# Kernel tuning notes

Measured on AMD Instinct MI355X. Metric: run time of the kernel, lower is better.

Reference implementation:

```python
import jax, jax.numpy as jnp
import numpy as np

DIM = 256
NUM_LAYERS = 64


def setup_inputs() -> dict:
    key = jax.random.key(0)
    kx, kt = jax.random.split(key)
    x = jax.random.normal(kx, (32768, DIM), dtype=jnp.float32)
    # theta[l, p]: scalar angle for pair p in layer l. Odd-offset layers use only
    # the first DIM//2 - 1 entries. Matches torch.randn(()) * pi init.
    theta = jax.random.normal(kt, (NUM_LAYERS, DIM // 2), dtype=jnp.float32) * jnp.pi
    return {"x": x, "theta": theta}


def _apply_layer(x, th, offset):
    """Apply one layer of 2x2 Givens-like rotations to pairs (i, i+1).

    U = [[c, s], [s, -c]] with c=cos(2*theta), s=sin(2*theta); U is symmetric so
    out = vec @ U.T = vec @ U -> yi = c*xi + s*xj, yj = s*xi - c*xj.
    """
    b, d = x.shape
    if offset == 0:
        npairs = d // 2
        c = jnp.cos(2.0 * th[:npairs])  # [npairs]
        s = jnp.sin(2.0 * th[:npairs])
        v = x.reshape(b, npairs, 2)
        xi, xj = v[..., 0], v[..., 1]
        yi = c * xi + s * xj
        yj = s * xi - c * xj
        return jnp.stack([yi, yj], axis=-1).reshape(b, d)
    else:
        npairs = d // 2 - 1
        c = jnp.cos(2.0 * th[:npairs])
        s = jnp.sin(2.0 * th[:npairs])
        inner = x[:, 1:d - 1].reshape(b, npairs, 2)
        xi, xj = inner[..., 0], inner[..., 1]
        yi = c * xi + s * xj
        yj = s * xi - c * xj
        mid = jnp.stack([yi, yj], axis=-1).reshape(b, d - 2)
        return jnp.concatenate([x[:, :1], mid, x[:, d - 1:]], axis=1)


def reference(x, theta):
    # Python loop over num_layers (fixed, small structural set).
    for depth in range(NUM_LAYERS):
        x = _apply_layer(x, theta[depth], depth % 2)
    return x
```

## Files before the change

### kernel.cpp

```cpp
#include <hip/hip_runtime.h>
#include <math.h>

#define DIM 256
#define NLAYERS 64

typedef __attribute__((ext_vector_type(8))) short short8;
typedef __attribute__((ext_vector_type(4))) float f32x4;

__device__ __forceinline__ float dpp_shl1_zero(float v) {
    int r = __builtin_amdgcn_update_dpp(0, __float_as_int(v), 0x130, 0xF, 0xF, true);
    return __int_as_float(r);
}
__device__ __forceinline__ float dpp_shr1_keep(float oldv, float v) {
    int r = __builtin_amdgcn_update_dpp(__float_as_int(oldv), __float_as_int(v), 0x138, 0xF, 0xF, false);
    return __int_as_float(r);
}
__device__ __forceinline__ unsigned short f2bf(float f) {
    unsigned u = __float_as_uint(f);
    u += 0x7FFFu + ((u >> 16) & 1u);
    return (unsigned short)(u >> 16);
}

__global__ __launch_bounds__(1024)
void build_m_kernel(const float* __restrict__ theta, unsigned short* __restrict__ bfrag) {
    __shared__ float tbl[NLAYERS * DIM];
    const int tid = threadIdx.x;
    #pragma unroll
    for (int kk = 0; kk < 8; ++kk) {
        int idx = tid + 1024 * kk;
        int l = idx >> 7, p = idx & 127;
        float s, c;
        sincosf(2.0f * theta[idx], &s, &c);
        if ((l & 1) && (p == 127)) { c = 1.0f; s = 0.0f; }
        tbl[idx * 2 + 0] = c;
        tbl[idx * 2 + 1] = s;
    }
    __syncthreads();

    const int w = tid >> 6;
    const int t = tid & 63;
    const int row = blockIdx.x * 16 + w;

    float e[4];
    #pragma unroll
    for (int j = 0; j < 4; ++j) e[j] = (4 * t + j == row) ? 1.0f : 0.0f;

    const float4* tbl4 = (const float4*)tbl;
    #pragma unroll 2
    for (int l = 0; l < NLAYERS; l += 2) {
        float4 cs = tbl4[(l << 6) + t];
        {
            float a0 = e[0], a1 = e[1], a2 = e[2], a3 = e[3];
            e[0] = cs.x * a0 + cs.y * a1;
            e[1] = cs.y * a0 - cs.x * a1;
            e[2] = cs.z * a2 + cs.w * a3;
            e[3] = cs.w * a2 - cs.z * a3;
        }
        float4 cs1 = tbl4[((l + 1) << 6) + t];
        {
            float a1 = e[1], a2 = e[2], a3 = e[3];
            float n1 = cs1.x * a1 + cs1.y * a2;
            float n2 = cs1.y * a1 - cs1.x * a2;
            float xjn = dpp_shl1_zero(e[0]);
            float n3  = cs1.z * a3 + cs1.w * xjn;
            float snd = cs1.w * a3 - cs1.z * xjn;
            e[0] = dpp_shr1_keep(e[0], snd);
            e[1] = n1; e[2] = n2; e[3] = n3;
        }
    }

    const int kt = row >> 5, g8 = (row >> 3) & 3, ki = row & 7;
    #pragma unroll
    for (int j = 0; j < 4; ++j) {
        int col = 4 * t + j;
        bfrag[(((col >> 4) * 8 + kt) * 64 + g8 * 16 + (col & 15)) * 8 + ki] = f2bf(e[j]);
    }
}

__global__ __launch_bounds__(512, 4)
void clements_gemm(const float* __restrict__ x,
                   const unsigned short* __restrict__ bfrag,
                   float* __restrict__ out) {
    __shared__ unsigned short afrag[2][4096];

    const int tid = threadIdx.x;
    const int w   = tid >> 6;
    const int t   = tid & 63;
    const int l16 = t & 15;
    const int g   = t >> 4;
    const long rowbase = (long)blockIdx.x * 64;

    const int sr  = tid >> 5;
    const int seg = tid & 31;
    const int q   = seg >> 2;
    const int sg  = seg & 3;
    const int wslot = (q * 64 + ((sg * 16 + sr) ^ q)) * 8;
    const float* xp = x + (rowbase + sr) * 256 + seg * 8;

    f32x4 pref[4][2];
#define LOADC(i) { pref[i][0] = *(const f32x4*)(xp + (i) * 16 * 256);      \
                   pref[i][1] = *(const f32x4*)(xp + (i) * 16 * 256 + 4); }
#define WRITEC(i) { short8 h;                                              \
        h[0]=f2bf(pref[i][0][0]); h[1]=f2bf(pref[i][0][1]);                \
        h[2]=f2bf(pref[i][0][2]); h[3]=f2bf(pref[i][0][3]);                \
        h[4]=f2bf(pref[i][1][0]); h[5]=f2bf(pref[i][1][1]);                \
        h[6]=f2bf(pref[i][1][2]); h[7]=f2bf(pref[i][1][3]);                \
        *(short8*)&afrag[(i) & 1][wslot] = h; }

    LOADC(0)
    LOADC(1)

    short8 Bf[8][2];
    {
        const short8* bp = (const short8*)bfrag;
        #pragma unroll
        for (int nt = 0; nt < 2; ++nt)
            #pragma unroll
            for (int kt = 0; kt < 8; ++kt)
                Bf[kt][nt] = bp[((w * 2 + nt) * 8 + kt) * 64 + t];
    }

    WRITEC(0)
    __syncthreads();

    #pragma unroll
    for (int i = 0; i < 4; ++i) {
        if (i + 2 < 4) LOADC(i + 2)

        f32x4 a0 = {0.f,0.f,0.f,0.f}, a1 = {0.f,0.f,0.f,0.f};
        #pragma unroll
        for (int kt = 0; kt < 8; ++kt) {
            short8 A = *(const short8*)&afrag[i & 1][(kt * 64 + (t ^ kt)) * 8];
            a0 = __builtin_amdgcn_mfma_f32_16x16x32_bf16(A, Bf[kt][0], a0, 0, 0, 0);
            a1 = __builtin_amdgcn_mfma_f32_16x16x32_bf16(A, Bf[kt][1], a1, 0, 0, 0);
        }
        float* o = out + (rowbase + i * 16 + g * 4) * 256 + 32 * w + l16;
        #pragma unroll
        for (int j = 0; j < 4; ++j) {
            o[(long)j * 256 +  0] = a0[j];
            o[(long)j * 256 + 16] = a1[j];
        }

        if (i + 1 < 4) { WRITEC(i + 1) __syncthreads(); }
    }
#undef LOADC
#undef WRITEC
}

__global__ __launch_bounds__(1024, 4)
void clements_direct(const float* __restrict__ x,
                     const float* __restrict__ theta,
                     float* __restrict__ out) {
    __shared__ float tbl[NLAYERS * DIM];
    const int tid = threadIdx.x;
    #pragma unroll
    for (int k = 0; k < 8; ++k) {
        int idx = tid + 1024 * k;
        int l = idx >> 7;
        int p = idx & 127;
        float s, c;
        sincosf(2.0f * theta[idx], &s, &c);
        if ((l & 1) && (p == 127)) { c = 1.0f; s = 0.0f; }
        tbl[idx * 2 + 0] = c;
        tbl[idx * 2 + 1] = s;
    }
    __syncthreads();
    const int w = tid >> 6;
    const int t = tid & 63;
    const long base = ((long)blockIdx.x * 16 + w) * 8;
    float e[8][4];
    #pragma unroll
    for (int r = 0; r < 8; ++r) {
        float4 v = ((const float4*)(x + (base + r) * (long)DIM))[t];
        e[r][0] = v.x; e[r][1] = v.y; e[r][2] = v.z; e[r][3] = v.w;
    }
    const float4* tbl4 = (const float4*)tbl;
    #pragma unroll 2
    for (int l = 0; l < NLAYERS; l += 2) {
        float4 cs = tbl4[(l << 6) + t];
        #pragma unroll
        for (int r = 0; r < 8; ++r) {
            float a0 = e[r][0], a1 = e[r][1], a2 = e[r][2], a3 = e[r][3];
            e[r][0] = cs.x * a0 + cs.y * a1;
            e[r][1] = cs.y * a0 - cs.x * a1;
            e[r][2] = cs.z * a2 + cs.w * a3;
            e[r][3] = cs.w * a2 - cs.z * a3;
        }
        float4 cs1 = tbl4[((l + 1) << 6) + t];
        #pragma unroll
        for (int r = 0; r < 8; ++r) {
            float a1 = e[r][1], a2 = e[r][2], a3 = e[r][3];
            float n1 = cs1.x * a1 + cs1.y * a2;
            float n2 = cs1.y * a1 - cs1.x * a2;
            float xjn = dpp_shl1_zero(e[r][0]);
            float n3  = cs1.z * a3 + cs1.w * xjn;
            float snd = cs1.w * a3 - cs1.z * xjn;
            e[r][0] = dpp_shr1_keep(e[r][0], snd);
            e[r][1] = n1; e[r][2] = n2; e[r][3] = n3;
        }
    }
    #pragma unroll
    for (int r = 0; r < 8; ++r) {
        float4 v;
        v.x = e[r][0]; v.y = e[r][1]; v.z = e[r][2]; v.w = e[r][3];
        ((float4*)(out + (base + r) * (long)DIM))[t] = v;
    }
}

extern "C" void kernel_launch(void* const* d_in, const int* in_sizes, int n_in,
                              void* d_out, int out_size, void* d_ws, size_t ws_size,
                              hipStream_t stream) {
    const float* x     = (const float*)d_in[0];
    const float* theta = (const float*)d_in[1];
    float* out = (float*)d_out;

    const size_t need = (size_t)DIM * DIM * sizeof(unsigned short);
    if (ws_size >= need) {
        unsigned short* bfrag = (unsigned short*)d_ws;
        hipLaunchKernelGGL(build_m_kernel, dim3(16),  dim3(1024), 0, stream, theta, bfrag);
        hipLaunchKernelGGL(clements_gemm,  dim3(512), dim3(512),  0, stream, x, bfrag, out);
    } else {
        hipLaunchKernelGGL(clements_direct, dim3(256), dim3(1024), 0, stream, x, theta, out);
    }
}
```

Baseline: 26.74 us.

## Stream x tiles directly into LDS via global_load_lds and convert at MFMA

```diff
diff --git a/kernel.cpp b/kernel.cpp
--- a/kernel.cpp
+++ b/kernel.cpp
@@ -20,17 +20,22 @@
     u += 0x7FFFu + ((u >> 16) & 1u);
     return (unsigned short)(u >> 16);
 }
-
-__global__ __launch_bounds__(1024)
+__device__ __forceinline__ unsigned cvtpk_bf16(float a, float b) {
+    unsigned r;
+    asm("v_cvt_pk_bf16_f32 %0, %1, %2" : "=v"(r) : "v"(a), "v"(b));
+    return r;
+}
+
+__global__ __launch_bounds__(256)
 void build_m_kernel(const float* __restrict__ theta, unsigned short* __restrict__ bfrag) {
     __shared__ float tbl[NLAYERS * DIM];
     const int tid = threadIdx.x;
-    #pragma unroll
-    for (int kk = 0; kk < 8; ++kk) {
-        int idx = tid + 1024 * kk;
+    #pragma unroll 4
+    for (int kk = 0; kk < 32; ++kk) {
+        int idx = tid + 256 * kk;
         int l = idx >> 7, p = idx & 127;
-        float s, c;
-        sincosf(2.0f * theta[idx], &s, &c);
+        float a = 2.0f * theta[idx];
+        float s = __sinf(a), c = __cosf(a);
         if ((l & 1) && (p == 127)) { c = 1.0f; s = 0.0f; }
         tbl[idx * 2 + 0] = c;
         tbl[idx * 2 + 1] = s;
@@ -39,7 +44,7 @@
 
     const int w = tid >> 6;
     const int t = tid & 63;
-    const int row = blockIdx.x * 16 + w;
+    const int row = blockIdx.x * 4 + w;
 
     float e[4];
     #pragma unroll
@@ -81,7 +86,7 @@
 void clements_gemm(const float* __restrict__ x,
                    const unsigned short* __restrict__ bfrag,
                    float* __restrict__ out) {
-    __shared__ unsigned short afrag[2][4096];
+    __shared__ float axf[4][16][64][4];
 
     const int tid = threadIdx.x;
     const int w   = tid >> 6;
@@ -90,26 +95,6 @@
     const int g   = t >> 4;
     const long rowbase = (long)blockIdx.x * 64;
 
-    const int sr  = tid >> 5;
-    const int seg = tid & 31;
-    const int q   = seg >> 2;
-    const int sg  = seg & 3;
-    const int wslot = (q * 64 + ((sg * 16 + sr) ^ q)) * 8;
-    const float* xp = x + (rowbase + sr) * 256 + seg * 8;
-
-    f32x4 pref[4][2];
-#define LOADC(i) { pref[i][0] = *(const f32x4*)(xp + (i) * 16 * 256);      \
-                   pref[i][1] = *(const f32x4*)(xp + (i) * 16 * 256 + 4); }
-#define WRITEC(i) { short8 h;                                              \
-        h[0]=f2bf(pref[i][0][0]); h[1]=f2bf(pref[i][0][1]);                \
-        h[2]=f2bf(pref[i][0][2]); h[3]=f2bf(pref[i][0][3]);                \
-        h[4]=f2bf(pref[i][1][0]); h[5]=f2bf(pref[i][1][1]);                \
-        h[6]=f2bf(pref[i][1][2]); h[7]=f2bf(pref[i][1][3]);                \
-        *(short8*)&afrag[(i) & 1][wslot] = h; }
-
-    LOADC(0)
-    LOADC(1)
-
     short8 Bf[8][2];
     {
         const short8* bp = (const short8*)bfrag;
@@ -119,20 +104,40 @@
             for (int kt = 0; kt < 8; ++kt)
                 Bf[kt][nt] = bp[((w * 2 + nt) * 8 + kt) * 64 + t];
     }
-
-    WRITEC(0)
-    __syncthreads();
-
-    #pragma unroll
-    for (int i = 0; i < 4; ++i) {
-        if (i + 2 < 4) LOADC(i + 2)
-
+    asm volatile("" ::: "memory");
+
+    const int r0 = 2 * w, r1 = 2 * w + 1;
+    const int gr0 = ((t & 48) | ((t ^ r0) & 15)) * 4;
+    const int gr1 = ((t & 48) | ((t ^ r1) & 15)) * 4;
+
+#define STAGE(i) { \
+    const float* g0 = x + (rowbase + (i) * 16 + r0) * 256 + gr0; \
+    const float* g1 = x + (rowbase + (i) * 16 + r1) * 256 + gr1; \
+    __builtin_amdgcn_global_load_lds((const __attribute__((address_space(1))) void*)g0, \
+        (__attribute__((address_space(3))) void*)&axf[i][r0][0][0], 16, 0, 0); \
+    __builtin_amdgcn_global_load_lds((const __attribute__((address_space(1))) void*)g1, \
+        (__attribute__((address_space(3))) void*)&axf[i][r1][0][0], 16, 0, 0); }
+
+#define GATE(n) { asm volatile("s_waitcnt vmcnt(" #n ")" ::: "memory"); \
+                  __builtin_amdgcn_s_barrier(); \
+                  __builtin_amdgcn_sched_barrier(0); }
+
+    auto compute = [&](int i) {
         f32x4 a0 = {0.f,0.f,0.f,0.f}, a1 = {0.f,0.f,0.f,0.f};
         #pragma unroll
         for (int kt = 0; kt < 8; ++kt) {
-            short8 A = *(const short8*)&afrag[i & 1][(kt * 64 + (t ^ kt)) * 8];
-            a0 = __builtin_amdgcn_mfma_f32_16x16x32_bf16(A, Bf[kt][0], a0, 0, 0, 0);
-            a1 = __builtin_amdgcn_mfma_f32_16x16x32_bf16(A, Bf[kt][1], a1, 0, 0, 0);
+            int j0 = kt * 8 + g * 2;
+            int s0 = (j0 & 48) | ((j0 ^ l16) & 15);
+            int s1 = ((j0 + 1) & 48) | (((j0 + 1) ^ l16) & 15);
+            f32x4 f0 = *(const f32x4*)&axf[i][l16][s0][0];
+            f32x4 f1 = *(const f32x4*)&axf[i][l16][s1][0];
+            union { short8 s; unsigned u[4]; } A;
+            A.u[0] = cvtpk_bf16(f0[0], f0[1]);
+            A.u[1] = cvtpk_bf16(f0[2], f0[3]);
+            A.u[2] = cvtpk_bf16(f1[0], f1[1]);
+            A.u[3] = cvtpk_bf16(f1[2], f1[3]);
+            a0 = __builtin_amdgcn_mfma_f32_16x16x32_bf16(A.s, Bf[kt][0], a0, 0, 0, 0);
+            a1 = __builtin_amdgcn_mfma_f32_16x16x32_bf16(A.s, Bf[kt][1], a1, 0, 0, 0);
         }
         float* o = out + (rowbase + i * 16 + g * 4) * 256 + 32 * w + l16;
         #pragma unroll
@@ -140,11 +145,16 @@
             o[(long)j * 256 +  0] = a0[j];
             o[(long)j * 256 + 16] = a1[j];
         }
-
-        if (i + 1 < 4) { WRITEC(i + 1) __syncthreads(); }
-    }
-#undef LOADC
-#undef WRITEC
+    };
+
+    STAGE(0) STAGE(1) STAGE(2)
+
+    GATE(4)  STAGE(3) compute(0);
+    GATE(12) compute(1);
+    GATE(18) compute(2);
+    GATE(16) compute(3);
+#undef STAGE
+#undef GATE
 }
 
 __global__ __launch_bounds__(1024, 4)
@@ -217,8 +227,8 @@
     const size_t need = (size_t)DIM * DIM * sizeof(unsigned short);
     if (ws_size >= need) {
         unsigned short* bfrag = (unsigned short*)d_ws;
-        hipLaunchKernelGGL(build_m_kernel, dim3(16),  dim3(1024), 0, stream, theta, bfrag);
-        hipLaunchKernelGGL(clements_gemm,  dim3(512), dim3(512),  0, stream, x, bfrag, out);
+        hipLaunchKernelGGL(build_m_kernel, dim3(64),  dim3(256), 0, stream, theta, bfrag);
+        hipLaunchKernelGGL(clements_gemm,  dim3(512), dim3(512), 0, stream, x, bfrag, out);
     } else {
         hipLaunchKernelGGL(clements_direct, dim3(256), dim3(1024), 0, stream, x, theta, out);
     }
```

After: 24.05 us. 10.1% less time.

## Deepen A-tile prefetch, use packed bf16 convert, new LDS swizzle and lighter barriers

Applied to the files above, without the earlier changes.

```diff
diff --git a/kernel.cpp b/kernel.cpp
--- a/kernel.cpp
+++ b/kernel.cpp
@@ -20,6 +20,11 @@
     u += 0x7FFFu + ((u >> 16) & 1u);
     return (unsigned short)(u >> 16);
 }
+__device__ __forceinline__ unsigned cvtpk_bf16(float a, float b) {
+    unsigned r;
+    asm("v_cvt_pk_bf16_f32 %0, %1, %2" : "=v"(r) : "v"(a), "v"(b));
+    return r;
+}
 
 __global__ __launch_bounds__(1024)
 void build_m_kernel(const float* __restrict__ theta, unsigned short* __restrict__ bfrag) {
@@ -29,8 +34,8 @@
     for (int kk = 0; kk < 8; ++kk) {
         int idx = tid + 1024 * kk;
         int l = idx >> 7, p = idx & 127;
-        float s, c;
-        sincosf(2.0f * theta[idx], &s, &c);
+        float a = 2.0f * theta[idx];
+        float s = __sinf(a), c = __cosf(a);
         if ((l & 1) && (p == 127)) { c = 1.0f; s = 0.0f; }
         tbl[idx * 2 + 0] = c;
         tbl[idx * 2 + 1] = s;
@@ -81,7 +86,7 @@
 void clements_gemm(const float* __restrict__ x,
                    const unsigned short* __restrict__ bfrag,
                    float* __restrict__ out) {
-    __shared__ unsigned short afrag[2][4096];
+    __shared__ unsigned short abf[4][4096];
 
     const int tid = threadIdx.x;
     const int w   = tid >> 6;
@@ -90,25 +95,24 @@
     const int g   = t >> 4;
     const long rowbase = (long)blockIdx.x * 64;
 
-    const int sr  = tid >> 5;
-    const int seg = tid & 31;
-    const int q   = seg >> 2;
-    const int sg  = seg & 3;
-    const int wslot = (q * 64 + ((sg * 16 + sr) ^ q)) * 8;
-    const float* xp = x + (rowbase + sr) * 256 + seg * 8;
-
-    f32x4 pref[4][2];
-#define LOADC(i) { pref[i][0] = *(const f32x4*)(xp + (i) * 16 * 256);      \
-                   pref[i][1] = *(const f32x4*)(xp + (i) * 16 * 256 + 4); }
-#define WRITEC(i) { short8 h;                                              \
-        h[0]=f2bf(pref[i][0][0]); h[1]=f2bf(pref[i][0][1]);                \
-        h[2]=f2bf(pref[i][0][2]); h[3]=f2bf(pref[i][0][3]);                \
-        h[4]=f2bf(pref[i][1][0]); h[5]=f2bf(pref[i][1][1]);                \
-        h[6]=f2bf(pref[i][1][2]); h[7]=f2bf(pref[i][1][3]);                \
-        *(short8*)&afrag[(i) & 1][wslot] = h; }
-
-    LOADC(0)
-    LOADC(1)
+    const int sr = tid >> 5;
+    const int so = tid & 31;
+    char* const wbase = (char*)&abf[0][0] +
+        ((((so >> 2) * 1024) + ((so & 3) * 256) + (sr * 16)) ^ ((so & 7) << 4));
+    const float* const xp = x + (rowbase + sr) * 256 + so * 8;
+
+    f32x4 pa[4], pb[4];
+#define LOADR(i) { pa[i] = *(const f32x4*)(xp + (i) * 16 * 256);       \
+                   pb[i] = *(const f32x4*)(xp + (i) * 16 * 256 + 4); }
+#define CVTW(i) { union { short8 s; unsigned u[4]; } h;                \
+        h.u[0] = cvtpk_bf16(pa[i][0], pa[i][1]);                       \
+        h.u[1] = cvtpk_bf16(pa[i][2], pa[i][3]);                       \
+        h.u[2] = cvtpk_bf16(pb[i][0], pb[i][1]);                       \
+        h.u[3] = cvtpk_bf16(pb[i][2], pb[i][3]);                       \
+        *(short8*)(wbase + (i) * 8192) = h.s; }
+#define BAR() { asm volatile("s_waitcnt lgkmcnt(0)" ::: "memory");     \
+                __builtin_amdgcn_s_barrier();                          \
+                __builtin_amdgcn_sched_barrier(0); }
 
     short8 Bf[8][2];
     {
@@ -120,17 +124,17 @@
                 Bf[kt][nt] = bp[((w * 2 + nt) * 8 + kt) * 64 + t];
     }
 
-    WRITEC(0)
-    __syncthreads();
-
-    #pragma unroll
-    for (int i = 0; i < 4; ++i) {
-        if (i + 2 < 4) LOADC(i + 2)
-
+    LOADR(0) LOADR(1) LOADR(2)
+    CVTW(0)
+    BAR()
+
+    const char* const rbase = (const char*)&abf[0][0];
+    auto compute = [&](int i) {
         f32x4 a0 = {0.f,0.f,0.f,0.f}, a1 = {0.f,0.f,0.f,0.f};
         #pragma unroll
         for (int kt = 0; kt < 8; ++kt) {
-            short8 A = *(const short8*)&afrag[i & 1][(kt * 64 + (t ^ kt)) * 8];
+            short8 A = *(const short8*)(rbase + (i) * 8192 +
+                ((kt * 1024 + t * 16) ^ (((kt * 4 + g) & 7) << 4)));
             a0 = __builtin_amdgcn_mfma_f32_16x16x32_bf16(A, Bf[kt][0], a0, 0, 0, 0);
             a1 = __builtin_amdgcn_mfma_f32_16x16x32_bf16(A, Bf[kt][1], a1, 0, 0, 0);
         }
@@ -140,11 +144,22 @@
             o[(long)j * 256 +  0] = a0[j];
             o[(long)j * 256 + 16] = a1[j];
         }
-
-        if (i + 1 < 4) { WRITEC(i + 1) __syncthreads(); }
-    }
-#undef LOADC
-#undef WRITEC
+    };
+
+    LOADR(3)
+    compute(0);
+    CVTW(1)
+    BAR()
+    compute(1);
+    CVTW(2)
+    BAR()
+    compute(2);
+    CVTW(3)
+    BAR()
+    compute(3);
+#undef LOADR
+#undef CVTW
+#undef BAR
 }
 
 __global__ __launch_bounds__(1024, 4)
```

Result: faster. 25.67 us (-4.0%).
